# Kernel tuning notes

Measured on AMD Instinct MI355X. Metric: run time of the kernel, lower is better.

## Reference

```python
import jax, jax.numpy as jnp
import numpy as np

NUM_VN = 4
HIDDEN = 64
N = 1_000_000
G = 8192


def setup_inputs() -> dict:
    key = jax.random.key(0)
    ks = jax.random.split(key, 8)
    node_feat = jax.random.normal(ks[0], (N, HIDDEN), dtype=jnp.float32)
    node_pos = jax.random.normal(ks[1], (N, 3), dtype=jnp.float32)
    vn_pos = jax.random.normal(ks[2], (G, 3 * NUM_VN), dtype=jnp.float32)
    batch = jnp.sort(jax.random.randint(ks[3], (N,), 0, G, dtype=jnp.int64))
    in_dim = NUM_VN ** 2  # 16
    s1 = 1.0 / np.sqrt(in_dim)
    s2 = 1.0 / np.sqrt(HIDDEN)
    W1 = jax.random.uniform(ks[4], (HIDDEN, in_dim), jnp.float32, -s1, s1)
    b1 = jax.random.uniform(ks[5], (HIDDEN,), jnp.float32, -s1, s1)
    W2 = jax.random.uniform(ks[6], (HIDDEN, HIDDEN), jnp.float32, -s2, s2)
    b2 = jax.random.uniform(ks[7], (HIDDEN,), jnp.float32, -s2, s2)
    return {"node_feat": node_feat, "node_pos": node_pos, "vn_pos": vn_pos,
            "batch": batch, "W1": W1, "b1": b1, "W2": W2, "b2": b2}


def _safe_cdist(v):
    # v: [N, num_vn, 3]; pairwise L2 distances -> [N, num_vn, num_vn]
    diff = v[:, :, None, :] - v[:, None, :, :]
    sq = jnp.sum(diff * diff, axis=-1)
    # sqrt with zero-safe gradient on the diagonal (matches torch.cdist grad=0 there)
    pos = sq > 0
    return jnp.where(pos, jnp.sqrt(jnp.where(pos, sq, 1.0)), 0.0)


def reference(node_feat, node_pos, vn_pos, batch, W1, b1, W2, b2):
    n = node_pos.shape[0]
    # gather per-node virtual-node positions, form relative vectors [N, num_vn, 3]
    info_vec = (jnp.tile(node_pos, (1, NUM_VN)) - vn_pos[batch]).reshape(n, NUM_VN, 3)
    info_scalar = _safe_cdist(info_vec).reshape(n, NUM_VN ** 2)
    norm = jnp.linalg.norm(info_scalar, axis=1, keepdims=True)
    info_scalar = info_scalar / (norm + 0.001)
    h = jax.nn.silu(info_scalar @ W1.T + b1)
    return h @ W2.T + b2
```

## Files before the change

### kernel.cpp

```cpp
#include <hip/hip_runtime.h>

#define LOG2E 1.44269504088896340736f

typedef __attribute__((ext_vector_type(8))) _Float16 half8;
typedef __attribute__((ext_vector_type(4))) float floatx4;

__global__ __launch_bounds__(256, 5) void vnmlp_mfma(
    const float* __restrict__ node_pos,
    const float* __restrict__ vn_pos,
    const void*  __restrict__ batch_raw,
    const float* __restrict__ W1,
    const float* __restrict__ b1,
    const float* __restrict__ W2,
    const float* __restrict__ b2,
    float*       __restrict__ out,
    int n)
{
    __shared__ _Float16 lds_h[256 * 64];

    const int t    = threadIdx.x;
    const int base = blockIdx.x * 256;
    const int i    = base + t;
    const int ic   = (i < n) ? i : (n - 1);
    const bool full = (base + 256 <= n);

    const int l  = t & 63;
    const int w  = t >> 6;
    const int lm = l & 15;
    const int q  = l >> 4;

    const int* b32 = (const int*)batch_raw;
    const int probe = b32[(n / 2) | 1] | b32[(n / 4) | 1] | b32[((n / 4) * 3) | 1];
    long long bi;
    if (probe == 0) bi = ((const long long*)batch_raw)[ic];
    else            bi = (long long)b32[ic];

    const float px = node_pos[3 * ic + 0];
    const float py = node_pos[3 * ic + 1];
    const float pz = node_pos[3 * ic + 2];

    const float4* vp4 = (const float4*)(vn_pos + 12 * bi);
    const float4 v0 = vp4[0], v1 = vp4[1], v2 = vp4[2];
    const float vx[4] = {px - v0.x, px - v0.w, px - v1.z, px - v2.y};
    const float vy[4] = {py - v0.y, py - v1.x, py - v1.w, py - v2.z};
    const float vz[4] = {pz - v0.z, pz - v1.y, pz - v2.x, pz - v2.w};

    float dn[6];
    float ss = 0.0f;
    {
        int p = 0;
#pragma unroll
        for (int a = 0; a < 4; ++a) {
#pragma unroll
            for (int k = a + 1; k < 4; ++k) {
                const float dx = vx[a] - vx[k];
                const float dy = vy[a] - vy[k];
                const float dz = vz[a] - vz[k];
                const float sq = dx * dx + dy * dy + dz * dz;
                dn[p++] = __builtin_amdgcn_sqrtf(sq);
                ss += sq;
            }
        }
    }
    ss *= 2.0f;
    const float inv = __builtin_amdgcn_rcpf(__builtin_amdgcn_sqrtf(ss) + 0.001f);
#pragma unroll
    for (int p = 0; p < 6; ++p) dn[p] *= inv;

    const int pa[6] = {0, 0, 0, 1, 1, 2};
    const int pb[6] = {1, 2, 3, 2, 3, 3};
#pragma unroll
    for (int c = 0; c < 8; ++c) {
        half8 v;
#pragma unroll
        for (int jj = 0; jj < 8; ++jj) {
            const int j = c * 8 + jj;
            float acc = b1[j];
#pragma unroll
            for (int p = 0; p < 6; ++p) {
                const float we = W1[j * 16 + pa[p] * 4 + pb[p]] + W1[j * 16 + pb[p] * 4 + pa[p]];
                acc = fmaf(dn[p], we, acc);
            }
            const float e = __builtin_amdgcn_exp2f(-LOG2E * acc);
            v[jj] = (_Float16)(acc * __builtin_amdgcn_rcpf(1.0f + e));
        }
        *(half8*)&lds_h[t * 64 + ((c ^ (t & 7)) * 8)] = v;
    }

    __asm__ volatile("s_waitcnt lgkmcnt(0)" ::: "memory");

    half8 Ah[4][2];
#pragma unroll
    for (int s = 0; s < 4; ++s) {
        const int nn = w * 64 + s * 16 + lm;
#pragma unroll
        for (int ks = 0; ks < 2; ++ks) {
            const int kc = ks * 4 + q;
            Ah[s][ks] = *(const half8*)&lds_h[nn * 64 + ((kc ^ (nn & 7)) * 8)];
        }
    }

#pragma unroll 1
    for (int c = 0; c < 4; ++c) {
        half8 Bh[2], Bl[2];
#pragma unroll
        for (int ks = 0; ks < 2; ++ks) {
            const float* wrow = W2 + (c * 16 + lm) * 64 + ks * 32 + q * 8;
            const floatx4 f0 = *(const floatx4*)(wrow);
            const floatx4 f1 = *(const floatx4*)(wrow + 4);
#pragma unroll
            for (int e = 0; e < 4; ++e) {
                const _Float16 h0 = (_Float16)f0[e];
                Bh[ks][e] = h0;
                Bl[ks][e] = (_Float16)(f0[e] - (float)h0);
                const _Float16 h1 = (_Float16)f1[e];
                Bh[ks][4 + e] = h1;
                Bl[ks][4 + e] = (_Float16)(f1[e] - (float)h1);
            }
        }
        const floatx4 bv = *(const floatx4*)(b2 + c * 16 + q * 4);

#pragma unroll
        for (int s = 0; s < 4; ++s) {
            floatx4 acc = bv;
#pragma unroll
            for (int ks = 0; ks < 2; ++ks) {
                acc = __builtin_amdgcn_mfma_f32_16x16x32_f16(Bh[ks], Ah[s][ks], acc, 0, 0, 0);
                acc = __builtin_amdgcn_mfma_f32_16x16x32_f16(Bl[ks], Ah[s][ks], acc, 0, 0, 0);
            }
            const int node = base + w * 64 + s * 16 + lm;
            if (full || node < n)
                *(floatx4*)(out + (size_t)node * 64 + c * 16 + q * 4) = acc;
        }
    }
}

extern "C" void kernel_launch(void* const* d_in, const int* in_sizes, int n_in,
                              void* d_out, int out_size, void* d_ws, size_t ws_size,
                              hipStream_t stream) {
    const float* node_pos = (const float*)d_in[1];
    const float* vn_pos   = (const float*)d_in[2];
    const void*  batch    = d_in[3];
    const float* W1       = (const float*)d_in[4];
    const float* b1       = (const float*)d_in[5];
    const float* W2       = (const float*)d_in[6];
    const float* b2       = (const float*)d_in[7];
    float* out = (float*)d_out;

    const int n = in_sizes[1] / 3;
    const int blocks = (n + 255) / 256;

    hipLaunchKernelGGL(vnmlp_mfma, dim3(blocks), dim3(256), 0, stream,
                       node_pos, vn_pos, batch, W1, b1, W2, b2, out, n);
}
```

Before: 467.5 us.

## Stage MFMA outputs through LDS for coalesced stores and hoist W2 conversion

Each wave now writes its MFMA results into its own swizzled LDS region, reusing the already-consumed activation tile space. It then reads them back so that every store instruction writes a contiguous 1KB run of output rows, instead of scattered 16-byte pieces spread over 16 rows. The W2 split into fp16 high and low parts, along with b2, is loaded once at kernel start rather than inside the column loop, and the loop order becomes rows-outer, columns-inner. Launch bounds drop from 5 to 4 waves per SIMD to make room for the extra registers these preloaded B fragments need. The cost is added LDS traffic and lower occupancy.

```diff
diff --git a/kernel.cpp b/kernel.cpp
--- a/kernel.cpp
+++ b/kernel.cpp
@@ -5,7 +5,7 @@
 typedef __attribute__((ext_vector_type(8))) _Float16 half8;
 typedef __attribute__((ext_vector_type(4))) float floatx4;
 
-__global__ __launch_bounds__(256, 5) void vnmlp_mfma(
+__global__ __launch_bounds__(256, 4) void vnmlp_mfma(
     const float* __restrict__ node_pos,
     const float* __restrict__ vn_pos,
     const void*  __restrict__ batch_raw,
@@ -28,6 +28,28 @@
     const int w  = t >> 6;
     const int lm = l & 15;
     const int q  = l >> 4;
+
+    half8 Bh[4][2], Bl[4][2];
+    floatx4 bv4[4];
+#pragma unroll
+    for (int c = 0; c < 4; ++c) {
+#pragma unroll
+        for (int ks = 0; ks < 2; ++ks) {
+            const float* wrow = W2 + (c * 16 + lm) * 64 + ks * 32 + q * 8;
+            const floatx4 f0 = *(const floatx4*)(wrow);
+            const floatx4 f1 = *(const floatx4*)(wrow + 4);
+#pragma unroll
+            for (int e = 0; e < 4; ++e) {
+                const _Float16 h0 = (_Float16)f0[e];
+                Bh[c][ks][e] = h0;
+                Bl[c][ks][e] = (_Float16)(f0[e] - (float)h0);
+                const _Float16 h1 = (_Float16)f1[e];
+                Bh[c][ks][4 + e] = h1;
+                Bl[c][ks][4 + e] = (_Float16)(f1[e] - (float)h1);
+            }
+        }
+        bv4[c] = *(const floatx4*)(b2 + c * 16 + q * 4);
+    }
 
     const int* b32 = (const int*)batch_raw;
     const int probe = b32[(n / 2) | 1] | b32[(n / 4) | 1] | b32[((n / 4) * 3) | 1];
@@ -89,48 +111,46 @@
 
     __asm__ volatile("s_waitcnt lgkmcnt(0)" ::: "memory");
 
-    half8 Ah[4][2];
-#pragma unroll
-    for (int s = 0; s < 4; ++s) {
-        const int nn = w * 64 + s * 16 + lm;
-#pragma unroll
-        for (int ks = 0; ks < 2; ++ks) {
-            const int kc = ks * 4 + q;
-            Ah[s][ks] = *(const half8*)&lds_h[nn * 64 + ((kc ^ (nn & 7)) * 8)];
-        }
-    }
+    char* wbytes = (char*)lds_h + w * 8192;
 
 #pragma unroll 1
-    for (int c = 0; c < 4; ++c) {
-        half8 Bh[2], Bl[2];
+    for (int sp = 0; sp < 2; ++sp) {
+        half8 Ah[2][2];
 #pragma unroll
-        for (int ks = 0; ks < 2; ++ks) {
-            const float* wrow = W2 + (c * 16 + lm) * 64 + ks * 32 + q * 8;
-            const floatx4 f0 = *(const floatx4*)(wrow);
-            const floatx4 f1 = *(const floatx4*)(wrow + 4);
+        for (int ss2 = 0; ss2 < 2; ++ss2) {
+            const int nn = w * 64 + (sp * 2 + ss2) * 16 + lm;
 #pragma unroll
-            for (int e = 0; e < 4; ++e) {
-                const _Float16 h0 = (_Float16)f0[e];
-                Bh[ks][e] = h0;
-                Bl[ks][e] = (_Float16)(f0[e] - (float)h0);
-                const _Float16 h1 = (_Float16)f1[e];
-                Bh[ks][4 + e] = h1;
-                Bl[ks][4 + e] = (_Float16)(f1[e] - (float)h1);
+            for (int ks = 0; ks < 2; ++ks) {
+                const int kc = ks * 4 + q;
+                Ah[ss2][ks] = *(const half8*)&lds_h[nn * 64 + ((kc ^ (nn & 7)) * 8)];
             }
         }
-        const floatx4 bv = *(const floatx4*)(b2 + c * 16 + q * 4);
 
 #pragma unroll
-        for (int s = 0; s < 4; ++s) {
-            floatx4 acc = bv;
+        for (int ss2 = 0; ss2 < 2; ++ss2) {
+            const int s = sp * 2 + ss2;
 #pragma unroll
-            for (int ks = 0; ks < 2; ++ks) {
-                acc = __builtin_amdgcn_mfma_f32_16x16x32_f16(Bh[ks], Ah[s][ks], acc, 0, 0, 0);
-                acc = __builtin_amdgcn_mfma_f32_16x16x32_f16(Bl[ks], Ah[s][ks], acc, 0, 0, 0);
+            for (int c = 0; c < 4; ++c) {
+                floatx4 acc = bv4[c];
+#pragma unroll
+                for (int ks = 0; ks < 2; ++ks) {
+                    acc = __builtin_amdgcn_mfma_f32_16x16x32_f16(Bh[c][ks], Ah[ss2][ks], acc, 0, 0, 0);
+                    acc = __builtin_amdgcn_mfma_f32_16x16x32_f16(Bl[c][ks], Ah[ss2][ks], acc, 0, 0, 0);
+                }
+                const int sb = (lm * 256 + c * 64 + q * 16) ^ ((lm & 7) << 4);
+                *(floatx4*)(wbytes + sb) = acc;
             }
-            const int node = base + w * 64 + s * 16 + lm;
-            if (full || node < n)
-                *(floatx4*)(out + (size_t)node * 64 + c * 16 + q * 4) = acc;
+            const int row0 = base + w * 64 + s * 16;
+            float* oreg = out + (size_t)row0 * 64;
+#pragma unroll
+            for (int r = 0; r < 4; ++r) {
+                const int g = r * 64 + l;
+                const int row_l = g >> 4;
+                const int rb = (g * 16) ^ ((row_l & 7) << 4);
+                const floatx4 v = *(const floatx4*)(wbytes + rb);
+                if (full || (row0 + row_l) < n)
+                    *(floatx4*)(oreg + g * 4) = v;
+            }
         }
     }
 }
```

Result: faster. 418.2 us (-10.5%).
